# Kernel optimization log

Hardware: AMD Instinct MI355X
Metric: run time of the kernel (lower is better)

The kernel has to match this reference:

```python
import jax, jax.numpy as jnp
import numpy as np

B, T, F = 2048, 128, 1
H1, H2 = 128, 64


def lstm_relu(x, W, U, b):
    """Keras LSTM with activation=relu, recurrent_activation=sigmoid.
    x: [B, T, Fin]; W: [Fin, 4H]; U: [H, 4H]; b: [4H]. Gate order i,f,g,o.
    Returns full sequence of hidden states [B, T, H]."""
    Bb = x.shape[0]
    H = U.shape[0]

    def step(carry, xt):
        h, c = carry
        z = xt @ W + h @ U + b  # [B, 4H]
        i, f, g, o = jnp.split(z, 4, axis=-1)
        i = jax.nn.sigmoid(i)
        f = jax.nn.sigmoid(f)
        o = jax.nn.sigmoid(o)
        g = jax.nn.relu(g)
        c = f * c + i * g
        h = o * jax.nn.relu(c)
        return (h, c), h

    h0 = jnp.zeros((Bb, H), x.dtype)
    (_, _), hs = jax.lax.scan(step, (h0, h0), jnp.swapaxes(x, 0, 1))
    return jnp.swapaxes(hs, 0, 1)  # [B, T, H]


def setup_inputs() -> dict:
    key = jax.random.key(0)
    ks = jax.random.split(key, 16)
    s = 0.05  # small init so relu LSTM stays numerically stable
    d = {
        "x": jax.random.normal(ks[0], (B, T, F), jnp.float32),
        "W1": jax.random.normal(ks[1], (F, 4 * H1), jnp.float32) * s,
        "U1": jax.random.normal(ks[2], (H1, 4 * H1), jnp.float32) * s,
        "b1": jnp.zeros((4 * H1,), jnp.float32),
        "W2": jax.random.normal(ks[3], (H1, 4 * H2), jnp.float32) * s,
        "U2": jax.random.normal(ks[4], (H2, 4 * H2), jnp.float32) * s,
        "b2": jnp.zeros((4 * H2,), jnp.float32),
        "W3": jax.random.normal(ks[5], (H2, 4 * H2), jnp.float32) * s,
        "U3": jax.random.normal(ks[6], (H2, 4 * H2), jnp.float32) * s,
        "b3": jnp.zeros((4 * H2,), jnp.float32),
        "W4": jax.random.normal(ks[7], (H2, 4 * H1), jnp.float32) * s,
        "U4": jax.random.normal(ks[8], (H1, 4 * H1), jnp.float32) * s,
        "b4": jnp.zeros((4 * H1,), jnp.float32),
        "Wd": jax.random.normal(ks[9], (H1, 1), jnp.float32) * s,
        "bd": jnp.zeros((1,), jnp.float32),
    }
    return d


def reference(x, W1, U1, b1, W2, U2, b2, W3, U3, b3, W4, U4, b4, Wd, bd):
    h = lstm_relu(x, W1, U1, b1)            # [B, T, 128]
    h = lstm_relu(h, W2, U2, b2)[:, -1]     # return_sequences=False -> [B, 64]
    h = jnp.broadcast_to(h[:, None, :], (h.shape[0], T, h.shape[-1]))  # RepeatVector
    h = lstm_relu(h, W3, U3, b3)            # [B, T, 64]
    h = lstm_relu(h, W4, U4, b4)            # [B, T, 128]
    out = h @ Wd + bd                       # TimeDistributed Dense(1) -> [B, T, 1]
    return out
```

## Files before the change

kernel.cpp:

```cpp
#include <hip/hip_runtime.h>


#define TSEQ 128
#define NTH  512
#define BSTR 408

typedef __attribute__((ext_vector_type(8))) short bf16x8;
typedef __attribute__((ext_vector_type(4))) float f32x4;
typedef __attribute__((ext_vector_type(2))) float f32x2;
typedef __attribute__((ext_vector_type(4))) short s16x4;
typedef unsigned short ushort_t;

#define FB_L1 0
#define FB_L2 256
#define FB_L3 448
#define FB_L4 512
#define FB_W3 896
#define WS_FRAGS 960
#define WS_NEEDED (WS_FRAGS * 1024)

__device__ __forceinline__ ushort_t f2bf(float f) {
    union { float f; unsigned u; } a; a.f = f;
    unsigned r = a.u + 0x7FFF + ((a.u >> 16) & 1);
    return (ushort_t)(r >> 16);
}
__device__ __forceinline__ float bf2f(ushort_t h) {
    union { unsigned u; float f; } a; a.u = ((unsigned)h) << 16;
    return a.f;
}
__device__ __forceinline__ float sigm(float z) { return 1.0f / (1.0f + __expf(-z)); }

__device__ __forceinline__ f32x4 MF(bf16x8 a, bf16x8 b, f32x4 c) {
    return __builtin_amdgcn_mfma_f32_16x16x32_bf16(a, b, c, 0, 0, 0);
}

__global__ void pack_weights(const float* __restrict__ U1, const float* __restrict__ W2,
                             const float* __restrict__ U2, const float* __restrict__ U3,
                             const float* __restrict__ W4, const float* __restrict__ U4,
                             const float* __restrict__ W3, ushort_t* __restrict__ out)
{
    const int f = blockIdx.x;
    const int lane = threadIdx.x;
    int fl, KT, ldm, ksplit = 1 << 30, ld2 = 0;
    const float *base, *base2 = nullptr;
    if (f < 256)      { fl = f;       KT = 4; ldm = 512; base = U1; }
    else if (f < 448) { fl = f - 256; KT = 6; ldm = 256; base = W2; ksplit = 128; base2 = U2; ld2 = 256; }
    else if (f < 512) { fl = f - 448; KT = 2; ldm = 256; base = U3; }
    else if (f < 896) { fl = f - 512; KT = 6; ldm = 512; base = W4; ksplit = 64;  base2 = U4; ld2 = 512; }
    else              { fl = f - 896; KT = 2; ldm = 256; base = W3; }
    const int jt = fl / (KT * 2);
    const int rem = fl % (KT * 2);
    const int kt = rem >> 1;
    const int s = rem & 1;
    const int j = jt * 16 + (lane & 15);
    ushort_t* o = out + f * 512 + lane * 8;
    #pragma unroll
    for (int i = 0; i < 8; ++i) {
        const int k = kt * 32 + (lane >> 4) * 8 + i;
        const float w = (k < ksplit) ? base[k * ldm + j] : base2[(k - ksplit) * ld2 + j];
        const ushort_t hi = f2bf(w);
        o[i] = s ? f2bf(w - bf2f(hi)) : hi;
    }
}

__global__ __launch_bounds__(NTH, 2) void lstm_mfma_kernel(
    const float* __restrict__ x,
    const float* __restrict__ W1, const float* __restrict__ b1,
    const float* __restrict__ b2, const float* __restrict__ b3,
    const float* __restrict__ b4,
    const float* __restrict__ Wd, const float* __restrict__ bd,
    const ushort_t* __restrict__ wsp,
    float* __restrict__ out)
{
    __shared__ __align__(16) ushort_t bU[16][BSTR];
    __shared__ __align__(16) float zb[16][260];
    __shared__ __align__(16) float z3x[16][260];
    __shared__ __align__(16) float c23[16][64];
    __shared__ __align__(16) float obuf[16][128];
    __shared__ __align__(16) float xls[16][132];
    __shared__ __align__(16) float w1ls[512], b1ls[512], b4ls[512], b2ls[256];

    const int tid  = threadIdx.x;
    const int wid  = tid >> 6;
    const int lane = tid & 63;
    const int quad = lane >> 4;
    const int l15  = lane & 15;
    const int r0   = blockIdx.x * 16;
    const bf16x8* A = (const bf16x8*)wsp;

    const int rg = tid >> 5;
    const int jp = (tid & 31) * 2;

    {
        unsigned* p = (unsigned*)&bU[0][0];
        for (int i = tid; i < 16 * BSTR / 2; i += NTH) p[i] = 0u;
        float* q = &c23[0][0];
        for (int i = tid; i < 16 * 64; i += NTH) q[i] = 0.f;
        const int srow = tid >> 5, scol = (tid & 31) * 4;
        *(f32x4*)&xls[srow][scol] = *(const f32x4*)&x[(r0 + srow) * TSEQ + scol];
        w1ls[tid] = W1[tid];
        b1ls[tid] = b1[tid];
        b4ls[tid] = b4[tid];
        if (tid < 256) b2ls[tid] = b2[tid];
    }

    const int hcb = 16 * wid + quad * 4;
    const float wd0 = Wd[lane], wd1 = Wd[64 + lane], bd0 = bd[0];

    float c1r[4] = {0.f, 0.f, 0.f, 0.f};
    float c4r[4] = {0.f, 0.f, 0.f, 0.f};

    __syncthreads();

    for (int t = 0; t < TSEQ; ++t) {
        const int rb1 = (t & 1) * 128, wb1 = 128 - rb1;

        {
            bf16x8 ah[16];
            #pragma unroll
            for (int q = 0; q < 4; ++q)
                #pragma unroll
                for (int kt = 0; kt < 4; ++kt)
                    ah[q * 4 + kt] = A[(FB_L1 + ((wid + 8 * q) * 4 + kt) * 2) * 64 + lane];
            bf16x8 Bh[4];
            #pragma unroll
            for (int kt = 0; kt < 4; ++kt)
                Bh[kt] = *(const bf16x8*)&bU[l15][rb1 + kt * 32 + quad * 8];
            const float xr = xls[l15][t];
            f32x4 acc[4];
            #pragma unroll
            for (int q = 0; q < 4; ++q) {
                const int jb = (wid + 8 * q) * 16 + quad * 4;
                f32x4 a = *(const f32x4*)&b1ls[jb];
                a += xr * *(const f32x4*)&w1ls[jb];
                #pragma unroll
                for (int kt = 0; kt < 4; ++kt)
                    a = MF(ah[q * 4 + kt], Bh[kt], a);
                acc[q] = a;
            }
            s16x4 hv;
            #pragma unroll
            for (int g = 0; g < 4; ++g) {
                const float zi = acc[0][g];
                const float zf = acc[1][g];
                const float zg = acc[2][g];
                const float zo = acc[3][g];
                const float c = sigm(zf) * c1r[g] + sigm(zi) * fmaxf(zg, 0.f);
                c1r[g] = c;
                const float h = sigm(zo) * fmaxf(c, 0.f);
                hv[g] = (short)f2bf(h);
            }
            *(s16x4*)&bU[l15][wb1 + hcb] = hv;
        }
        __syncthreads();

        {
            bf16x8 ah[12];
            #pragma unroll
            for (int jj = 0; jj < 2; ++jj)
                #pragma unroll
                for (int kt = 0; kt < 6; ++kt)
                    ah[jj * 6 + kt] = A[(FB_L2 + ((2 * wid + jj) * 6 + kt) * 2) * 64 + lane];
            bf16x8 Bh[6];
            #pragma unroll
            for (int kt = 0; kt < 4; ++kt)
                Bh[kt] = *(const bf16x8*)&bU[l15][wb1 + kt * 32 + quad * 8];
            #pragma unroll
            for (int kt = 4; kt < 6; ++kt)
                Bh[kt] = *(const bf16x8*)&bU[l15][256 + (kt - 4) * 32 + quad * 8];
            #pragma unroll
            for (int jj = 0; jj < 2; ++jj) {
                const int jt = 2 * wid + jj;
                f32x4 a = *(const f32x4*)&b2ls[jt * 16 + quad * 4];
                #pragma unroll
                for (int kt = 0; kt < 6; ++kt)
                    a = MF(ah[jj * 6 + kt], Bh[kt], a);
                *(f32x4*)&zb[l15][jt * 16 + quad * 4] = a;
            }
        }
        __syncthreads();

        {
            const f32x2 zi = *(const f32x2*)&zb[rg][jp];
            const f32x2 zf = *(const f32x2*)&zb[rg][64 + jp];
            const f32x2 zg = *(const f32x2*)&zb[rg][128 + jp];
            const f32x2 zo = *(const f32x2*)&zb[rg][192 + jp];
            f32x2 c = *(const f32x2*)&c23[rg][jp];
            unsigned hw = 0;
            #pragma unroll
            for (int k = 0; k < 2; ++k) {
                const float cc = sigm(zf[k]) * c[k] + sigm(zi[k]) * fmaxf(zg[k], 0.f);
                c[k] = cc;
                const float h = sigm(zo[k]) * fmaxf(cc, 0.f);
                hw |= ((unsigned)f2bf(h)) << (16 * k);
            }
            *(f32x2*)&c23[rg][jp] = c;
            *(unsigned*)&bU[rg][256 + jp] = hw;
        }
    }
    __syncthreads();

    {
        bf16x8 Bh[2];
        #pragma unroll
        for (int kt = 0; kt < 2; ++kt)
            Bh[kt] = *(const bf16x8*)&bU[l15][256 + kt * 32 + quad * 8];
        #pragma unroll
        for (int jj = 0; jj < 2; ++jj) {
            const int jt = 2 * wid + jj;
            f32x4 a = *(const f32x4*)&b3[jt * 16 + quad * 4];
            #pragma unroll
            for (int kt = 0; kt < 2; ++kt) {
                const bf16x8 ah = A[(FB_W3 + (jt * 2 + kt) * 2) * 64 + lane];
                a = MF(ah, Bh[kt], a);
            }
            *(f32x4*)&z3x[l15][jt * 16 + quad * 4] = a;
        }
    }
    __syncthreads();
    {
        unsigned* p = (unsigned*)&bU[0][0];
        for (int i = tid; i < 16 * BSTR / 2; i += NTH) p[i] = 0u;
        float* q = &c23[0][0];
        for (int i = tid; i < 16 * 64; i += NTH) q[i] = 0.f;
        c4r[0] = c4r[1] = c4r[2] = c4r[3] = 0.f;
    }
    __syncthreads();

    for (int t = 0; t < TSEQ; ++t) {
        const int rb3 = (t & 1) * 64, wb3 = 64 - rb3;
        const int rb4 = 128 + (t & 1) * 128;
        const int wb4 = (rb4 == 128) ? 256 : 128;

        {
            bf16x8 ah[4];
            #pragma unroll
            for (int jj = 0; jj < 2; ++jj)
                #pragma unroll
                for (int kt = 0; kt < 2; ++kt)
                    ah[jj * 2 + kt] = A[(FB_L3 + ((2 * wid + jj) * 2 + kt) * 2) * 64 + lane];
            bf16x8 Bh[2];
            #pragma unroll
            for (int kt = 0; kt < 2; ++kt)
                Bh[kt] = *(const bf16x8*)&bU[l15][rb3 + kt * 32 + quad * 8];
            #pragma unroll
            for (int jj = 0; jj < 2; ++jj) {
                const int jt = 2 * wid + jj;
                f32x4 a = {0.f, 0.f, 0.f, 0.f};
                #pragma unroll
                for (int kt = 0; kt < 2; ++kt)
                    a = MF(ah[jj * 2 + kt], Bh[kt], a);
                *(f32x4*)&zb[l15][jt * 16 + quad * 4] = a;
            }
        }
        __syncthreads();

        {
            const f32x2 zi = *(const f32x2*)&zb[rg][jp]       + *(const f32x2*)&z3x[rg][jp];
            const f32x2 zf = *(const f32x2*)&zb[rg][64 + jp]  + *(const f32x2*)&z3x[rg][64 + jp];
            const f32x2 zg = *(const f32x2*)&zb[rg][128 + jp] + *(const f32x2*)&z3x[rg][128 + jp];
            const f32x2 zo = *(const f32x2*)&zb[rg][192 + jp] + *(const f32x2*)&z3x[rg][192 + jp];
            f32x2 c = *(const f32x2*)&c23[rg][jp];
            unsigned hw = 0;
            #pragma unroll
            for (int k = 0; k < 2; ++k) {
                const float cc = sigm(zf[k]) * c[k] + sigm(zi[k]) * fmaxf(zg[k], 0.f);
                c[k] = cc;
                const float h = sigm(zo[k]) * fmaxf(cc, 0.f);
                hw |= ((unsigned)f2bf(h)) << (16 * k);
            }
            *(f32x2*)&c23[rg][jp] = c;
            *(unsigned*)&bU[rg][wb3 + jp] = hw;

            if (t > 0) {
                #pragma unroll
                for (int e = 0; e < 2; ++e) {
                    const int r = wid + 8 * e;
                    const float h0 = bf2f(bU[r][rb4 + lane]);
                    const float h1_ = bf2f(bU[r][rb4 + 64 + lane]);
                    float v = h0 * wd0 + h1_ * wd1;
                    v += __shfl_down(v, 32);
                    v += __shfl_down(v, 16);
                    v += __shfl_down(v, 8);
                    v += __shfl_down(v, 4);
                    v += __shfl_down(v, 2);
                    v += __shfl_down(v, 1);
                    if (lane == 0) obuf[r][t - 1] = v + bd0;
                }
            }
        }
        __syncthreads();

        {
            bf16x8 Bh[6];
            #pragma unroll
            for (int kt = 0; kt < 2; ++kt)
                Bh[kt] = *(const bf16x8*)&bU[l15][wb3 + kt * 32 + quad * 8];
            #pragma unroll
            for (int kt = 2; kt < 6; ++kt)
                Bh[kt] = *(const bf16x8*)&bU[l15][rb4 + (kt - 2) * 32 + quad * 8];
            bf16x8 ah[24];
            #pragma unroll
            for (int q = 0; q < 4; ++q)
                #pragma unroll
                for (int kt = 0; kt < 6; ++kt)
                    ah[q * 6 + kt] = A[(FB_L4 + ((wid + 8 * q) * 6 + kt) * 2) * 64 + lane];
            f32x4 acc[4];
            #pragma unroll
            for (int q = 0; q < 4; ++q) {
                f32x4 a = *(const f32x4*)&b4ls[(wid + 8 * q) * 16 + quad * 4];
                #pragma unroll
                for (int kt = 0; kt < 6; ++kt)
                    a = MF(ah[q * 6 + kt], Bh[kt], a);
                acc[q] = a;
            }
            s16x4 hv;
            #pragma unroll
            for (int g = 0; g < 4; ++g) {
                const float zi = acc[0][g];
                const float zf = acc[1][g];
                const float zg = acc[2][g];
                const float zo = acc[3][g];
                const float c = sigm(zf) * c4r[g] + sigm(zi) * fmaxf(zg, 0.f);
                c4r[g] = c;
                const float h = sigm(zo) * fmaxf(c, 0.f);
                hv[g] = (short)f2bf(h);
            }
            *(s16x4*)&bU[l15][wb4 + hcb] = hv;
        }
    }
    __syncthreads();
    {
        #pragma unroll
        for (int e = 0; e < 2; ++e) {
            const int r = wid + 8 * e;
            const float h0 = bf2f(bU[r][128 + lane]);
            const float h1_ = bf2f(bU[r][128 + 64 + lane]);
            float v = h0 * wd0 + h1_ * wd1;
            v += __shfl_down(v, 32);
            v += __shfl_down(v, 16);
            v += __shfl_down(v, 8);
            v += __shfl_down(v, 4);
            v += __shfl_down(v, 2);
            v += __shfl_down(v, 1);
            if (lane == 0) obuf[r][127] = v + bd0;
        }
    }
    __syncthreads();
    {
        const int frow = tid >> 5;
        const int fcol = (tid & 31) * 4;
        *(f32x4*)&out[(r0 + frow) * TSEQ + fcol] = *(const f32x4*)&obuf[frow][fcol];
    }
}

#define FNT 512
#define FRPB 8
__global__ __launch_bounds__(FNT, 2) void lstm_stack_kernel(
    const float* __restrict__ x,
    const float* __restrict__ W1, const float* __restrict__ U1, const float* __restrict__ b1,
    const float* __restrict__ W2, const float* __restrict__ U2, const float* __restrict__ b2,
    const float* __restrict__ W3, const float* __restrict__ U3, const float* __restrict__ b3,
    const float* __restrict__ W4, const float* __restrict__ U4, const float* __restrict__ b4,
    const float* __restrict__ Wd, const float* __restrict__ bd,
    float* __restrict__ out)
{
    __shared__ float h1s[FRPB][128], c1s[FRPB][128];
    __shared__ float h2s[FRPB][64],  c2s[FRPB][64];
    __shared__ float h3s[FRPB][64],  c3s[FRPB][64];
    __shared__ float h4s[FRPB][128], c4s[FRPB][128];
    __shared__ float zbf[FRPB][512];
    __shared__ float z3xf[FRPB][256];
    __shared__ float xs[FRPB];

    const int tid = threadIdx.x;
    const int r0  = blockIdx.x * FRPB;
    const int jg  = tid & 255;
    const int grp = tid >> 8;
    const int rb  = grp * 4;

    {
        float* p1 = &h1s[0][0]; float* p2 = &c1s[0][0];
        float* p3 = &h4s[0][0]; float* p4 = &c4s[0][0];
        for (int i = tid; i < FRPB * 128; i += FNT) { p1[i]=0.f; p2[i]=0.f; p3[i]=0.f; p4[i]=0.f; }
        float* q1 = &h2s[0][0]; float* q2 = &c2s[0][0];
        float* q3 = &h3s[0][0]; float* q4 = &c3s[0][0];
        for (int i = tid; i < FRPB * 64; i += FNT) { q1[i]=0.f; q2[i]=0.f; q3[i]=0.f; q4[i]=0.f; }
    }
    __syncthreads();

    const float w1j = W1[tid];
    const float b1j = b1[tid];
    const float b2j = b2[jg];

    for (int t = 0; t < TSEQ; ++t) {
        if (tid < FRPB) xs[tid] = x[(r0 + tid) * TSEQ + t];
        __syncthreads();
        {
            float acc[FRPB];
            #pragma unroll
            for (int r = 0; r < FRPB; ++r) acc[r] = 0.f;
            const float* Uc = U1 + tid;
            #pragma unroll 4
            for (int k4 = 0; k4 < 32; ++k4) {
                const float u0 = Uc[(k4*4+0)*512];
                const float u1 = Uc[(k4*4+1)*512];
                const float u2 = Uc[(k4*4+2)*512];
                const float u3 = Uc[(k4*4+3)*512];
                #pragma unroll
                for (int r = 0; r < FRPB; ++r) {
                    const float4 h = ((const float4*)h1s[r])[k4];
                    acc[r] += h.x*u0 + h.y*u1 + h.z*u2 + h.w*u3;
                }
            }
            #pragma unroll
            for (int r = 0; r < FRPB; ++r) zbf[r][tid] = acc[r] + xs[r]*w1j + b1j;
        }
        __syncthreads();
        for (int e = tid; e < FRPB * 128; e += FNT) {
            const int r = e >> 7, hc = e & 127;
            const float zi = zbf[r][hc], zf = zbf[r][128+hc], zg = zbf[r][256+hc], zo = zbf[r][384+hc];
            const float c = sigm(zf)*c1s[r][hc] + sigm(zi)*fmaxf(zg, 0.f);
            c1s[r][hc] = c;
            h1s[r][hc] = sigm(zo)*fmaxf(c, 0.f);
        }
        __syncthreads();
        {
            float acc[4] = {0.f, 0.f, 0.f, 0.f};
            const float* Wc = W2 + jg;
            #pragma unroll 4
            for (int k4 = 0; k4 < 32; ++k4) {
                const float u0 = Wc[(k4*4+0)*256];
                const float u1 = Wc[(k4*4+1)*256];
                const float u2 = Wc[(k4*4+2)*256];
                const float u3 = Wc[(k4*4+3)*256];
                #pragma unroll
                for (int q = 0; q < 4; ++q) {
                    const float4 h = ((const float4*)h1s[rb+q])[k4];
                    acc[q] += h.x*u0 + h.y*u1 + h.z*u2 + h.w*u3;
                }
            }
            const float* Uc = U2 + jg;
            #pragma unroll 4
            for (int k4 = 0; k4 < 16; ++k4) {
                const float u0 = Uc[(k4*4+0)*256];
                const float u1 = Uc[(k4*4+1)*256];
                const float u2 = Uc[(k4*4+2)*256];
                const float u3 = Uc[(k4*4+3)*256];
                #pragma unroll
                for (int q = 0; q < 4; ++q) {
                    const float4 h = ((const float4*)h2s[rb+q])[k4];
                    acc[q] += h.x*u0 + h.y*u1 + h.z*u2 + h.w*u3;
                }
            }
            #pragma unroll
            for (int q = 0; q < 4; ++q) zbf[rb+q][jg] = acc[q] + b2j;
        }
        __syncthreads();
        {
            const int r = tid >> 6, hc = tid & 63;
            const float zi = zbf[r][hc], zf = zbf[r][64+hc], zg = zbf[r][128+hc], zo = zbf[r][192+hc];
            const float c = sigm(zf)*c2s[r][hc] + sigm(zi)*fmaxf(zg, 0.f);
            c2s[r][hc] = c;
            h2s[r][hc] = sigm(zo)*fmaxf(c, 0.f);
        }
        __syncthreads();
    }
    {
        float acc[4] = {0.f, 0.f, 0.f, 0.f};
        const float* Wc = W3 + jg;
        #pragma unroll 4
        for (int k4 = 0; k4 < 16; ++k4) {
            const float u0 = Wc[(k4*4+0)*256];
            const float u1 = Wc[(k4*4+1)*256];
            const float u2 = Wc[(k4*4+2)*256];
            const float u3 = Wc[(k4*4+3)*256];
            #pragma unroll
            for (int q = 0; q < 4; ++q) {
                const float4 h = ((const float4*)h2s[rb+q])[k4];
                acc[q] += h.x*u0 + h.y*u1 + h.z*u2 + h.w*u3;
            }
        }
        const float b3j = b3[jg];
        #pragma unroll
        for (int q = 0; q < 4; ++q) z3xf[rb+q][jg] = acc[q] + b3j;
    }
    __syncthreads();

    const float b4j = b4[tid];
    const float wd0 = Wd[tid & 63];
    const float wd1 = Wd[64 + (tid & 63)];
    const float bd0 = bd[0];

    for (int t = 0; t < TSEQ; ++t) {
        {
            float acc[4];
            #pragma unroll
            for (int q = 0; q < 4; ++q) acc[q] = z3xf[rb+q][jg];
            const float* Uc = U3 + jg;
            #pragma unroll 4
            for (int k4 = 0; k4 < 16; ++k4) {
                const float u0 = Uc[(k4*4+0)*256];
                const float u1 = Uc[(k4*4+1)*256];
                const float u2 = Uc[(k4*4+2)*256];
                const float u3 = Uc[(k4*4+3)*256];
                #pragma unroll
                for (int q = 0; q < 4; ++q) {
                    const float4 h = ((const float4*)h3s[rb+q])[k4];
                    acc[q] += h.x*u0 + h.y*u1 + h.z*u2 + h.w*u3;
                }
            }
            #pragma unroll
            for (int q = 0; q < 4; ++q) zbf[rb+q][jg] = acc[q];
        }
        __syncthreads();
        {
            const int r = tid >> 6, hc = tid & 63;
            const float zi = zbf[r][hc], zf = zbf[r][64+hc], zg = zbf[r][128+hc], zo = zbf[r][192+hc];
            const float c = sigm(zf)*c3s[r][hc] + sigm(zi)*fmaxf(zg, 0.f);
            c3s[r][hc] = c;
            h3s[r][hc] = sigm(zo)*fmaxf(c, 0.f);
        }
        __syncthreads();
        {
            float acc[FRPB];
            #pragma unroll
            for (int r = 0; r < FRPB; ++r) acc[r] = 0.f;
            const float* Wc = W4 + tid;
            #pragma unroll 4
            for (int k4 = 0; k4 < 16; ++k4) {
                const float u0 = Wc[(k4*4+0)*512];
                const float u1 = Wc[(k4*4+1)*512];
                const float u2 = Wc[(k4*4+2)*512];
                const float u3 = Wc[(k4*4+3)*512];
                #pragma unroll
                for (int r = 0; r < FRPB; ++r) {
                    const float4 h = ((const float4*)h3s[r])[k4];
                    acc[r] += h.x*u0 + h.y*u1 + h.z*u2 + h.w*u3;
                }
            }
            const float* Uc = U4 + tid;
            #pragma unroll 4
            for (int k4 = 0; k4 < 32; ++k4) {
                const float u0 = Uc[(k4*4+0)*512];
                const float u1 = Uc[(k4*4+1)*512];
                const float u2 = Uc[(k4*4+2)*512];
                const float u3 = Uc[(k4*4+3)*512];
                #pragma unroll
                for (int r = 0; r < FRPB; ++r) {
                    const float4 h = ((const float4*)h4s[r])[k4];
                    acc[r] += h.x*u0 + h.y*u1 + h.z*u2 + h.w*u3;
                }
            }
            #pragma unroll
            for (int r = 0; r < FRPB; ++r) zbf[r][tid] = acc[r] + b4j;
        }
        __syncthreads();
        for (int e = tid; e < FRPB * 128; e += FNT) {
            const int r = e >> 7, hc = e & 127;
            const float zi = zbf[r][hc], zf = zbf[r][128+hc], zg = zbf[r][256+hc], zo = zbf[r][384+hc];
            const float c = sigm(zf)*c4s[r][hc] + sigm(zi)*fmaxf(zg, 0.f);
            c4s[r][hc] = c;
            h4s[r][hc] = sigm(zo)*fmaxf(c, 0.f);
        }
        __syncthreads();
        {
            const int wv = tid >> 6, ln = tid & 63;
            float v = h4s[wv][ln]*wd0 + h4s[wv][64+ln]*wd1;
            v += __shfl_down(v, 32, 64);
            v += __shfl_down(v, 16, 64);
            v += __shfl_down(v,  8, 64);
            v += __shfl_down(v,  4, 64);
            v += __shfl_down(v,  2, 64);
            v += __shfl_down(v,  1, 64);
            if (ln == 0) out[(r0 + wv) * TSEQ + t] = v + bd0;
        }
    }
}

extern "C" void kernel_launch(void* const* d_in, const int* in_sizes, int n_in,
                              void* d_out, int out_size, void* d_ws, size_t ws_size,
                              hipStream_t stream) {
    const float* x  = (const float*)d_in[0];
    const float* W1 = (const float*)d_in[1];
    const float* U1 = (const float*)d_in[2];
    const float* b1 = (const float*)d_in[3];
    const float* W2 = (const float*)d_in[4];
    const float* U2 = (const float*)d_in[5];
    const float* b2 = (const float*)d_in[6];
    const float* W3 = (const float*)d_in[7];
    const float* U3 = (const float*)d_in[8];
    const float* b3 = (const float*)d_in[9];
    const float* W4 = (const float*)d_in[10];
    const float* U4 = (const float*)d_in[11];
    const float* b4 = (const float*)d_in[12];
    const float* Wd = (const float*)d_in[13];
    const float* bd = (const float*)d_in[14];
    float* out = (float*)d_out;

    if (ws_size >= (size_t)WS_NEEDED) {
        ushort_t* wsp = (ushort_t*)d_ws;
        pack_weights<<<dim3(WS_FRAGS), dim3(64), 0, stream>>>(U1, W2, U2, U3, W4, U4, W3, wsp);
        lstm_mfma_kernel<<<dim3(2048 / 16), dim3(NTH), 0, stream>>>(
            x, W1, b1, b2, b3, b4, Wd, bd, wsp, out);
    } else {
        lstm_stack_kernel<<<dim3(2048 / FRPB), dim3(FNT), 0, stream>>>(
            x, W1, U1, b1, W2, U2, b2, W3, U3, b3, W4, U4, b4, Wd, bd, out);
    }
}
```

Baseline: 612.7 us.

## Prefetch next-stage MFMA weight fragments from global across barriers in LSTM loops

Result: slower. 700.4 us (+14.3%).

```diff
diff --git a/kernel.cpp b/kernel.cpp
--- a/kernel.cpp
+++ b/kernel.cpp
@@ -4,6 +4,8 @@
 #define TSEQ 128
 #define NTH  512
 #define BSTR 408
+
+#define BAR() asm volatile("s_waitcnt lgkmcnt(0)\n\ts_barrier" ::: "memory")
 
 typedef __attribute__((ext_vector_type(8))) short bf16x8;
 typedef __attribute__((ext_vector_type(4))) float f32x4;
@@ -63,7 +65,7 @@
     }
 }
 
-__global__ __launch_bounds__(NTH, 2) void lstm_mfma_kernel(
+__global__ __launch_bounds__(NTH, 1) void lstm_mfma_kernel(
     const float* __restrict__ x,
     const float* __restrict__ W1, const float* __restrict__ b1,
     const float* __restrict__ b2, const float* __restrict__ b3,
@@ -110,18 +112,20 @@
     float c1r[4] = {0.f, 0.f, 0.f, 0.f};
     float c4r[4] = {0.f, 0.f, 0.f, 0.f};
 
+    bf16x8 pf1[16];
+    #pragma unroll
+    for (int q = 0; q < 4; ++q)
+        #pragma unroll
+        for (int kt = 0; kt < 4; ++kt)
+            pf1[q * 4 + kt] = A[(FB_L1 + ((wid + 8 * q) * 4 + kt) * 2) * 64 + lane];
+
     __syncthreads();
 
     for (int t = 0; t < TSEQ; ++t) {
         const int rb1 = (t & 1) * 128, wb1 = 128 - rb1;
-
-        {
-            bf16x8 ah[16];
-            #pragma unroll
-            for (int q = 0; q < 4; ++q)
-                #pragma unroll
-                for (int kt = 0; kt < 4; ++kt)
-                    ah[q * 4 + kt] = A[(FB_L1 + ((wid + 8 * q) * 4 + kt) * 2) * 64 + lane];
+        bf16x8 pf2[12];
+
+        {
             bf16x8 Bh[4];
             #pragma unroll
             for (int kt = 0; kt < 4; ++kt)
@@ -135,9 +139,14 @@
                 a += xr * *(const f32x4*)&w1ls[jb];
                 #pragma unroll
                 for (int kt = 0; kt < 4; ++kt)
-                    a = MF(ah[q * 4 + kt], Bh[kt], a);
+                    a = MF(pf1[q * 4 + kt], Bh[kt], a);
                 acc[q] = a;
             }
+            #pragma unroll
+            for (int jj = 0; jj < 2; ++jj)
+                #pragma unroll
+                for (int kt = 0; kt < 6; ++kt)
+                    pf2[jj * 6 + kt] = A[(FB_L2 + ((2 * wid + jj) * 6 + kt) * 2) * 64 + lane];
             s16x4 hv;
             #pragma unroll
             for (int g = 0; g < 4; ++g) {
@@ -152,15 +161,9 @@
             }
             *(s16x4*)&bU[l15][wb1 + hcb] = hv;
         }
-        __syncthreads();
-
-        {
-            bf16x8 ah[12];
-            #pragma unroll
-            for (int jj = 0; jj < 2; ++jj)
-                #pragma unroll
-                for (int kt = 0; kt < 6; ++kt)
-                    ah[jj * 6 + kt] = A[(FB_L2 + ((2 * wid + jj) * 6 + kt) * 2) * 64 + lane];
+        BAR();
+
+        {
             bf16x8 Bh[6];
             #pragma unroll
             for (int kt = 0; kt < 4; ++kt)
@@ -174,11 +177,16 @@
                 f32x4 a = *(const f32x4*)&b2ls[jt * 16 + quad * 4];
                 #pragma unroll
                 for (int kt = 0; kt < 6; ++kt)
-                    a = MF(ah[jj * 6 + kt], Bh[kt], a);
+                    a = MF(pf2[jj * 6 + kt], Bh[kt], a);
                 *(f32x4*)&zb[l15][jt * 16 + quad * 4] = a;
             }
-        }
-        __syncthreads();
+            #pragma unroll
+            for (int q = 0; q < 4; ++q)
+                #pragma unroll
+                for (int kt = 0; kt < 4; ++kt)
+                    pf1[q * 4 + kt] = A[(FB_L1 + ((wid + 8 * q) * 4 + kt) * 2) * 64 + lane];
+        }
+        BAR();
 
         {
             const f32x2 zi = *(const f32x2*)&zb[rg][jp];
@@ -225,20 +233,21 @@
         for (int i = tid; i < 16 * 64; i += NTH) q[i] = 0.f;
         c4r[0] = c4r[1] = c4r[2] = c4r[3] = 0.f;
     }
+    bf16x8 pf3[4];
+    #pragma unroll
+    for (int jj = 0; jj < 2; ++jj)
+        #pragma unroll
+        for (int kt = 0; kt < 2; ++kt)
+            pf3[jj * 2 + kt] = A[(FB_L3 + ((2 * wid + jj) * 2 + kt) * 2) * 64 + lane];
     __syncthreads();
 
     for (int t = 0; t < TSEQ; ++t) {
         const int rb3 = (t & 1) * 64, wb3 = 64 - rb3;
         const int rb4 = 128 + (t & 1) * 128;
         const int wb4 = (rb4 == 128) ? 256 : 128;
-
-        {
-            bf16x8 ah[4];
-            #pragma unroll
-            for (int jj = 0; jj < 2; ++jj)
-                #pragma unroll
-                for (int kt = 0; kt < 2; ++kt)
-                    ah[jj * 2 + kt] = A[(FB_L3 + ((2 * wid + jj) * 2 + kt) * 2) * 64 + lane];
+        bf16x8 pf4[24];
+
+        {
             bf16x8 Bh[2];
             #pragma unroll
             for (int kt = 0; kt < 2; ++kt)
@@ -249,11 +258,16 @@
                 f32x4 a = {0.f, 0.f, 0.f, 0.f};
                 #pragma unroll
                 for (int kt = 0; kt < 2; ++kt)
-                    a = MF(ah[jj * 2 + kt], Bh[kt], a);
+                    a = MF(pf3[jj * 2 + kt], Bh[kt], a);
                 *(f32x4*)&zb[l15][jt * 16 + quad * 4] = a;
             }
-        }
-        __syncthreads();
+            #pragma unroll
+            for (int q = 0; q < 4; ++q)
+                #pragma unroll
+                for (int kt = 0; kt < 6; ++kt)
+                    pf4[q * 6 + kt] = A[(FB_L4 + ((wid + 8 * q) * 6 + kt) * 2) * 64 + lane];
+        }
+        BAR();
 
         {
             const f32x2 zi = *(const f32x2*)&zb[rg][jp]       + *(const f32x2*)&z3x[rg][jp];
@@ -289,7 +303,7 @@
                 }
             }
         }
-        __syncthreads();
+        BAR();
 
         {
             bf16x8 Bh[6];
@@ -299,21 +313,20 @@
             #pragma unroll
             for (int kt = 2; kt < 6; ++kt)
                 Bh[kt] = *(const bf16x8*)&bU[l15][rb4 + (kt - 2) * 32 + quad * 8];
-            bf16x8 ah[24];
-            #pragma unroll
-            for (int q = 0; q < 4; ++q)
-                #pragma unroll
-                for (int kt = 0; kt < 6; ++kt)
-                    ah[q * 6 + kt] = A[(FB_L4 + ((wid + 8 * q) * 6 + kt) * 2) * 64 + lane];
             f32x4 acc[4];
             #pragma unroll
             for (int q = 0; q < 4; ++q) {
                 f32x4 a = *(const f32x4*)&b4ls[(wid + 8 * q) * 16 + quad * 4];
                 #pragma unroll
                 for (int kt = 0; kt < 6; ++kt)
-                    a = MF(ah[q * 6 + kt], Bh[kt], a);
+                    a = MF(pf4[q * 6 + kt], Bh[kt], a);
                 acc[q] = a;
             }
+            #pragma unroll
+            for (int jj = 0; jj < 2; ++jj)
+                #pragma unroll
+                for (int kt = 0; kt < 2; ++kt)
+                    pf3[jj * 2 + kt] = A[(FB_L3 + ((2 * wid + jj) * 2 + kt) * 2) * 64 + lane];
             s16x4 hv;
             #pragma unroll
             for (int g = 0; g < 4; ++g) {
```
